# Kernel optimization log

Measured on AMD Instinct MI355X. Metric: run time of the kernel, lower is better.

The kernel has to match this reference:

```python
import jax, jax.numpy as jnp
import numpy as np

N_NODES = 100000


def gcn_conv(x, src, dst, W, b):
    # PyG GCNConv: linear transform first, then symmetric-normalized aggregation.
    h = x @ W  # [N, out]
    ones = jnp.ones(dst.shape[0], dtype=x.dtype)
    deg = jax.ops.segment_sum(ones, dst, num_segments=N_NODES)  # in-degree incl. self-loops
    dinv = jnp.where(deg > 0, jax.lax.rsqrt(deg), 0.0)
    norm = dinv[src] * dinv[dst]  # [E]
    msg = h[src] * norm[:, None]  # gather + scale
    out = jax.ops.segment_sum(msg, dst, num_segments=N_NODES)  # scatter-add
    return out + b


def add_self_loops(edge_index):
    loops = jnp.arange(N_NODES, dtype=edge_index.dtype)
    src = jnp.concatenate([edge_index[0], loops])
    dst = jnp.concatenate([edge_index[1], loops])
    return src, dst


def setup_inputs() -> dict:
    key = jax.random.key(0)
    k1, k2, k3, k4 = jax.random.split(key, 4)
    N, F, H, C, E = N_NODES, 512, 16, 40, 3200000
    x = jax.random.normal(k1, (N, F), dtype=jnp.float32)
    edge_index = jax.random.randint(k2, (2, E), 0, N, dtype=jnp.int64)
    W1 = jax.random.normal(k3, (F, H), dtype=jnp.float32) * (1.0 / np.sqrt(F))
    b1 = jnp.zeros((H,), dtype=jnp.float32)
    W2 = jax.random.normal(k4, (H, C), dtype=jnp.float32) * (1.0 / np.sqrt(H))
    b2 = jnp.zeros((C,), dtype=jnp.float32)
    return {"x": x, "edge_index": edge_index, "W1": W1, "b1": b1, "W2": W2, "b2": b2}


def reference(x, edge_index, W1, b1, W2, b2):
    src, dst = add_self_loops(edge_index)
    h = gcn_conv(x, src, dst, W1, b1)
    h = jax.nn.relu(h)
    logits = gcn_conv(h, src, dst, W2, b2)
    return jax.nn.log_softmax(logits, axis=1), logits
```

## Files before the change

### kernel.cpp

```cpp
#include <hip/hip_runtime.h>
#include <hip/hip_bf16.h>
#include <math.h>

#define N_NODES 100000
#define F_IN 512
#define H_DIM 16
#define C_DIM 40

#define BSHIFT 9
#define BNODES 512
#define NBUCK 196
#define CHUNK 8192
#define SRC_MASK 0x1FFFF
#define SORT_CAP 18432

#define KSPLIT 4
#define KSEG (F_IN / KSPLIT)


__global__ void __launch_bounds__(256) bhist_kernel(const int* __restrict__ dst,
                                                    int* __restrict__ BC, int E) {
    __shared__ int cnt[NBUCK];
    int start = blockIdx.x * CHUNK;
    int end = start + CHUNK < E ? start + CHUNK : E;
    for (int i = threadIdx.x; i < NBUCK; i += 256) cnt[i] = 0;
    __syncthreads();
    for (int i = start + threadIdx.x; i < end; i += 256)
        atomicAdd(&cnt[dst[i] >> BSHIFT], 1);
    __syncthreads();
    for (int i = threadIdx.x; i < NBUCK; i += 256) {
        int c = cnt[i];
        if (c) atomicAdd(&BC[i], c);
    }
}


__global__ void __launch_bounds__(256) bscan_kernel(const int* __restrict__ BC,
                                                    int* __restrict__ BO,
                                                    int* __restrict__ cursor,
                                                    int* __restrict__ R, int E, int N) {
    __shared__ int buf[2][256];
    int tid = threadIdx.x;
    int v = (tid < NBUCK) ? BC[tid] : 0;
    int cur = 0;
    buf[0][tid] = v;
    __syncthreads();
    for (int off = 1; off < 256; off <<= 1) {
        int t = buf[cur][tid] + ((tid >= off) ? buf[cur][tid - off] : 0);
        cur ^= 1;
        buf[cur][tid] = t;
        __syncthreads();
    }
    int excl = buf[cur][tid] - v;
    if (tid <= NBUCK) {
        BO[tid] = excl;
        if (tid < NBUCK) cursor[tid] = excl;
    }
    if (tid == 0) R[N] = E;
}


__global__ void __launch_bounds__(256) partition_kernel(const int* __restrict__ src,
                                                        const int* __restrict__ dst,
                                                        int* __restrict__ cursor,
                                                        int* __restrict__ packed, int E) {
    __shared__ int cnt[NBUCK];
    __shared__ int base[NBUCK];
    __shared__ int lpre[NBUCK + 1];
    __shared__ int sbuf[2][256];
    __shared__ int stage[CHUNK];
    int tid = threadIdx.x;
    int start = blockIdx.x * CHUNK;
    int end = start + CHUNK < E ? start + CHUNK : E;
    int nch = end - start;
    for (int i = tid; i < NBUCK; i += 256) cnt[i] = 0;
    __syncthreads();
    for (int i = start + tid; i < end; i += 256)
        atomicAdd(&cnt[dst[i] >> BSHIFT], 1);
    __syncthreads();
    int v = (tid < NBUCK) ? cnt[tid] : 0;
    int cur = 0;
    sbuf[0][tid] = v;
    __syncthreads();
    for (int off = 1; off < 256; off <<= 1) {
        int t = sbuf[cur][tid] + ((tid >= off) ? sbuf[cur][tid - off] : 0);
        cur ^= 1;
        sbuf[cur][tid] = t;
        __syncthreads();
    }
    if (tid < NBUCK) {
        lpre[tid] = sbuf[cur][tid] - v;
        base[tid] = v ? atomicAdd(&cursor[tid], v) : 0;
        cnt[tid] = 0;
    }
    if (tid == 0) lpre[NBUCK] = nch;
    __syncthreads();
    for (int i = start + tid; i < end; i += 256) {
        int d = dst[i];
        int b = d >> BSHIFT;
        int p = lpre[b] + atomicAdd(&cnt[b], 1);
        stage[p] = ((d & (BNODES - 1)) << 17) | src[i];
    }
    __syncthreads();
    for (int j = tid; j < nch; j += 256) {
        int loB = 0, hiB = NBUCK;
        while (hiB - loB > 1) {
            int mid = (loB + hiB) >> 1;
            if (lpre[mid] <= j) loB = mid; else hiB = mid;
        }
        packed[base[loB] + (j - lpre[loB])] = stage[j];
    }
}


__global__ void __launch_bounds__(1024) sort2_kernel(const int* __restrict__ BO,
                                                     const int* __restrict__ packed,
                                                     int* __restrict__ R,
                                                     float* __restrict__ dinv,
                                                     int* __restrict__ eidx, int N) {
    __shared__ int cnt[BNODES];
    __shared__ int buf[2][BNODES];
    __shared__ int stage[SORT_CAP];
    int b = blockIdx.x;
    int tid = threadIdx.x;
    int lo = BO[b], hi = BO[b + 1];
    int len = hi - lo;
    if (tid < BNODES) cnt[tid] = 0;
    __syncthreads();
    for (int e = lo + tid; e < hi; e += 1024)
        atomicAdd(&cnt[packed[e] >> 17], 1);
    __syncthreads();
    int deg = (tid < BNODES) ? cnt[tid] : 0;
    int cur = 0;
    if (tid < BNODES) buf[0][tid] = deg;
    __syncthreads();
    for (int off = 1; off < BNODES; off <<= 1) {
        int t = 0;
        if (tid < BNODES) t = buf[cur][tid] + ((tid >= off) ? buf[cur][tid - off] : 0);
        cur ^= 1;
        if (tid < BNODES) buf[cur][tid] = t;
        __syncthreads();
    }
    if (tid < BNODES) {
        int excl = buf[cur][tid] - deg;
        int n = (b << BSHIFT) + tid;
        if (n < N) {
            R[n] = lo + excl;
            dinv[n] = rsqrtf((float)(deg + 1));
        }
        cnt[tid] = excl;
    }
    __syncthreads();
    if (len <= SORT_CAP) {
        for (int e = lo + tid; e < hi; e += 1024) {
            int p = packed[e];
            int pos = atomicAdd(&cnt[p >> 17], 1);
            stage[pos] = p & SRC_MASK;
        }
        __syncthreads();
        for (int j = tid; j < len; j += 1024) eidx[lo + j] = stage[j];
    } else {
        for (int e = lo + tid; e < hi; e += 1024) {
            int p = packed[e];
            int pos = atomicAdd(&cnt[p >> 17], 1);
            eidx[lo + pos] = p & SRC_MASK;
        }
    }
}


#define G1_ISSUE(BUF, G)                                             \
    {                                                                \
        _Pragma("unroll")                                            \
        for (int p = 0; p < 8; ++p) BUF[p] = xr[(G) * 8 + p];        \
    }

#define G1_COMPUTE(BUF, G)                                           \
    {                                                                \
        const float* xf = (const float*)(BUF);                       \
        _Pragma("unroll")                                            \
        for (int j = 0; j < 32; ++j) {                               \
            float s = xf[j];                                         \
            const float4* Wj = (const float4*)(Wb + ((G) * 32 + j) * H_DIM); \
            _Pragma("unroll")                                        \
            for (int p = 0; p < 4; ++p) {                            \
                float4 wv = Wj[p];                                   \
                acc[4 * p + 0] += s * wv.x;                          \
                acc[4 * p + 1] += s * wv.y;                          \
                acc[4 * p + 2] += s * wv.z;                          \
                acc[4 * p + 3] += s * wv.w;                          \
            }                                                        \
        }                                                            \
    }

__global__ void __launch_bounds__(256) gemm1p_kernel(const float* __restrict__ x,
                                                     const float* __restrict__ W1,
                                                     float* __restrict__ part, int N) {
    int bid = blockIdx.x;
    int ks = bid & (KSPLIT - 1);
    int rb = bid >> 2;
    int row = rb * 256 + threadIdx.x;
    int cr = row < N ? row : N - 1;
    const float4* xr = (const float4*)(x + (size_t)cr * F_IN + ks * KSEG);
    const float* Wb = W1 + ks * KSEG * H_DIM;

    float4 bufA[8], bufB[8];
    float acc[H_DIM];
#pragma unroll
    for (int k = 0; k < H_DIM; k++) acc[k] = 0.0f;

    G1_ISSUE(bufA, 0);
    G1_ISSUE(bufB, 1);
    G1_COMPUTE(bufA, 0);
    G1_ISSUE(bufA, 2);
    G1_COMPUTE(bufB, 1);
    G1_ISSUE(bufB, 3);
    G1_COMPUTE(bufA, 2);
    G1_COMPUTE(bufB, 3);

    if (row < N) {
        float4* o = (float4*)(part + (size_t)ks * N * H_DIM + (size_t)row * H_DIM);
#pragma unroll
        for (int p = 0; p < 4; p++)
            o[p] = make_float4(acc[4 * p], acc[4 * p + 1], acc[4 * p + 2], acc[4 * p + 3]);
    }
}


__global__ void __launch_bounds__(256) g1red_kernel(const float* __restrict__ part,
                                                    const float* __restrict__ dinv,
                                                    float* __restrict__ g1, int N) {
    int t = blockIdx.x * 256 + threadIdx.x;
    int total = N * H_DIM / 4;
    if (t >= total) return;
    const float4* p = (const float4*)part;
    float4 a = p[t];
    float4 b = p[t + (size_t)total];
    float4 c = p[t + (size_t)2 * total];
    float4 d = p[t + (size_t)3 * total];
    float di = dinv[t >> 2];
    ((float4*)g1)[t] = make_float4(di * (((a.x + b.x) + c.x) + d.x),
                                   di * (((a.y + b.y) + c.y) + d.y),
                                   di * (((a.z + b.z) + c.z) + d.z),
                                   di * (((a.w + b.w) + c.w) + d.w));
}


__global__ void __launch_bounds__(256) agg1_kernel(const int* __restrict__ R,
                                                   const int* __restrict__ eidx,
                                                   const float* __restrict__ g1,
                                                   const float* __restrict__ dinv,
                                                   const float* __restrict__ b1,
                                                   float* __restrict__ g2, int N) {
    int t = blockIdx.x * 256 + threadIdx.x;
    int n = t >> 4;
    if (n >= N) return;
    int k = t & 15;
    int lo = R[n], hi = R[n + 1];
    float sum = g1[t];
    int e = lo;
    for (; e + 8 <= hi; e += 8) {
        int s[8];
        float v[8];
#pragma unroll
        for (int u = 0; u < 8; u++) s[u] = eidx[e + u];
#pragma unroll
        for (int u = 0; u < 8; u++) v[u] = g1[s[u] * H_DIM + k];
#pragma unroll
        for (int u = 0; u < 8; u++) sum += v[u];
    }
    for (; e < hi; ++e) sum += g1[eidx[e] * H_DIM + k];
    float di = dinv[n];
    g2[t] = di * fmaxf(di * sum + b1[k], 0.0f);
}


__global__ void __launch_bounds__(256) fin2_kernel(const int* __restrict__ R,
                                                   const int* __restrict__ eidx,
                                                   const float* __restrict__ g2,
                                                   const float* __restrict__ dinv,
                                                   const float* __restrict__ W2,
                                                   const float* __restrict__ b2,
                                                   float* __restrict__ out, int N) {
    __shared__ float w2s[H_DIM * C_DIM];
    __shared__ float b2s[C_DIM];
    __shared__ float vsh[16][17];
    for (int i = threadIdx.x; i < H_DIM * C_DIM; i += 256) w2s[i] = W2[i];
    if (threadIdx.x < C_DIM) b2s[threadIdx.x] = b2[threadIdx.x];

    int t = blockIdx.x * 256 + threadIdx.x;
    int n = t >> 4;
    int k = t & 15;
    int lo = R[n], hi = R[n + 1];
    float sum = g2[t];
    int e = lo;
    for (; e + 8 <= hi; e += 8) {
        int s[8];
        float v[8];
#pragma unroll
        for (int u = 0; u < 8; u++) s[u] = eidx[e + u];
#pragma unroll
        for (int u = 0; u < 8; u++) v[u] = g2[s[u] * H_DIM + k];
#pragma unroll
        for (int u = 0; u < 8; u++) sum += v[u];
    }
    for (; e < hi; ++e) sum += g2[eidx[e] * H_DIM + k];
    vsh[threadIdx.x >> 4][k] = dinv[n] * sum;
    __syncthreads();

    int g = threadIdx.x >> 4;
    int j = threadIdx.x & 15;
    const float* v = vsh[g];
    int c2 = (j < 8) ? 32 + j : j;
    float lg0 = b2s[j];
    float lg1 = b2s[j + 16];
    float lg2 = (j < 8) ? b2s[32 + j] : -1e30f;
    float lg2acc = 0.0f;
#pragma unroll
    for (int kk = 0; kk < H_DIM; ++kk) {
        float vk = v[kk];
        lg0 += vk * w2s[kk * C_DIM + j];
        lg1 += vk * w2s[kk * C_DIM + j + 16];
        lg2acc += vk * w2s[kk * C_DIM + c2];
    }
    if (j < 8) lg2 += lg2acc;

    float m = fmaxf(fmaxf(lg0, lg1), lg2);
#pragma unroll
    for (int s = 1; s < 16; s <<= 1) m = fmaxf(m, __shfl_xor(m, s, 64));
    float ss = __expf(lg0 - m) + __expf(lg1 - m) + ((j < 8) ? __expf(lg2 - m) : 0.0f);
#pragma unroll
    for (int s = 1; s < 16; s <<= 1) ss += __shfl_xor(ss, s, 64);
    float lse = m + __logf(ss);

    size_t base = (size_t)n * C_DIM;
    size_t lim = (size_t)N * C_DIM;
    out[base + j] = lg0 - lse;
    out[base + 16 + j] = lg1 - lse;
    if (j < 8) out[base + 32 + j] = lg2 - lse;
    out[lim + base + j] = lg0;
    out[lim + base + 16 + j] = lg1;
    if (j < 8) out[lim + base + 32 + j] = lg2;
}


extern "C" void kernel_launch(void* const* d_in, const int* in_sizes, int n_in,
                              void* d_out, int out_size, void* d_ws, size_t ws_size,
                              hipStream_t stream) {
    const float* x  = (const float*)d_in[0];
    const int* ei   = (const int*)d_in[1];
    const float* W1 = (const float*)d_in[2];
    const float* b1 = (const float*)d_in[3];
    const float* W2 = (const float*)d_in[4];
    const float* b2 = (const float*)d_in[5];
    float* out = (float*)d_out;

    const int N = N_NODES;
    const int E = in_sizes[1] / 2;
    const int* src = ei;
    const int* dst = ei + E;

    int* R      = (int*)d_ws;
    int* BC     = R + 100016;
    int* BO     = BC + 512;
    int* cursor = BO + 256;
    float* dinv = (float*)(cursor + 256);
    int* eidx   = (int*)(dinv + 100016);
    int* packed = eidx + E;
    float* g1   = (float*)packed;
    float* g2   = g1 + 16 * N;
    float* part = g2 + 16 * N;

    const int NB = (N + 255) / 256;
    const int NCH = (E + CHUNK - 1) / CHUNK;

    hipMemsetAsync(BC, 0, NBUCK * sizeof(int), stream);
    bhist_kernel<<<NCH, 256, 0, stream>>>(dst, BC, E);
    bscan_kernel<<<1, 256, 0, stream>>>(BC, BO, cursor, R, E, N);
    partition_kernel<<<NCH, 256, 0, stream>>>(src, dst, cursor, packed, E);
    sort2_kernel<<<NBUCK, 1024, 0, stream>>>(BO, packed, R, dinv, eidx, N);

    gemm1p_kernel<<<NB * KSPLIT, 256, 0, stream>>>(x, W1, part, N);
    g1red_kernel<<<(N * H_DIM / 4 + 255) / 256, 256, 0, stream>>>(part, dinv, g1, N);
    agg1_kernel<<<(N * 16 + 255) / 256, 256, 0, stream>>>(R, eidx, g1, dinv, b1, g2, N);
    fin2_kernel<<<N / 16, 256, 0, stream>>>(R, eidx, g2, dinv, W2, b2, out, N);
}
```

Baseline: 518.2 us.

## Merge partition with GEMM and sort with reduction, using fixed-capacity buckets

Drops the separate histogram and scan passes by giving each destination bucket a fixed-capacity region (CAP slots), so the partition step can claim offsets directly through atomic cursors. The partition and the x@W1 split-K GEMM now run as one launch using disjoint block ranges, and the per-bucket sort is fused with the partial-sum reduction, so independent work overlaps and the launch count drops. Because dinv is no longer ready when g1 is reduced, agg1 now gathers dinv per neighbour and applies it there, and R2 stores explicit row ends since rows are no longer contiguous. The cost is an extra dinv gather per edge in agg1 and a silent correctness risk if any bucket receives more edges than CAP.

```diff
diff --git a/kernel.cpp b/kernel.cpp
--- a/kernel.cpp
+++ b/kernel.cpp
@@ -10,163 +10,13 @@
 #define BSHIFT 9
 #define BNODES 512
 #define NBUCK 196
-#define CHUNK 8192
+#define CHUNK4 4096
 #define SRC_MASK 0x1FFFF
+#define CAP 20480
 #define SORT_CAP 18432
 
 #define KSPLIT 4
 #define KSEG (F_IN / KSPLIT)
-
-
-__global__ void __launch_bounds__(256) bhist_kernel(const int* __restrict__ dst,
-                                                    int* __restrict__ BC, int E) {
-    __shared__ int cnt[NBUCK];
-    int start = blockIdx.x * CHUNK;
-    int end = start + CHUNK < E ? start + CHUNK : E;
-    for (int i = threadIdx.x; i < NBUCK; i += 256) cnt[i] = 0;
-    __syncthreads();
-    for (int i = start + threadIdx.x; i < end; i += 256)
-        atomicAdd(&cnt[dst[i] >> BSHIFT], 1);
-    __syncthreads();
-    for (int i = threadIdx.x; i < NBUCK; i += 256) {
-        int c = cnt[i];
-        if (c) atomicAdd(&BC[i], c);
-    }
-}
-
-
-__global__ void __launch_bounds__(256) bscan_kernel(const int* __restrict__ BC,
-                                                    int* __restrict__ BO,
-                                                    int* __restrict__ cursor,
-                                                    int* __restrict__ R, int E, int N) {
-    __shared__ int buf[2][256];
-    int tid = threadIdx.x;
-    int v = (tid < NBUCK) ? BC[tid] : 0;
-    int cur = 0;
-    buf[0][tid] = v;
-    __syncthreads();
-    for (int off = 1; off < 256; off <<= 1) {
-        int t = buf[cur][tid] + ((tid >= off) ? buf[cur][tid - off] : 0);
-        cur ^= 1;
-        buf[cur][tid] = t;
-        __syncthreads();
-    }
-    int excl = buf[cur][tid] - v;
-    if (tid <= NBUCK) {
-        BO[tid] = excl;
-        if (tid < NBUCK) cursor[tid] = excl;
-    }
-    if (tid == 0) R[N] = E;
-}
-
-
-__global__ void __launch_bounds__(256) partition_kernel(const int* __restrict__ src,
-                                                        const int* __restrict__ dst,
-                                                        int* __restrict__ cursor,
-                                                        int* __restrict__ packed, int E) {
-    __shared__ int cnt[NBUCK];
-    __shared__ int base[NBUCK];
-    __shared__ int lpre[NBUCK + 1];
-    __shared__ int sbuf[2][256];
-    __shared__ int stage[CHUNK];
-    int tid = threadIdx.x;
-    int start = blockIdx.x * CHUNK;
-    int end = start + CHUNK < E ? start + CHUNK : E;
-    int nch = end - start;
-    for (int i = tid; i < NBUCK; i += 256) cnt[i] = 0;
-    __syncthreads();
-    for (int i = start + tid; i < end; i += 256)
-        atomicAdd(&cnt[dst[i] >> BSHIFT], 1);
-    __syncthreads();
-    int v = (tid < NBUCK) ? cnt[tid] : 0;
-    int cur = 0;
-    sbuf[0][tid] = v;
-    __syncthreads();
-    for (int off = 1; off < 256; off <<= 1) {
-        int t = sbuf[cur][tid] + ((tid >= off) ? sbuf[cur][tid - off] : 0);
-        cur ^= 1;
-        sbuf[cur][tid] = t;
-        __syncthreads();
-    }
-    if (tid < NBUCK) {
-        lpre[tid] = sbuf[cur][tid] - v;
-        base[tid] = v ? atomicAdd(&cursor[tid], v) : 0;
-        cnt[tid] = 0;
-    }
-    if (tid == 0) lpre[NBUCK] = nch;
-    __syncthreads();
-    for (int i = start + tid; i < end; i += 256) {
-        int d = dst[i];
-        int b = d >> BSHIFT;
-        int p = lpre[b] + atomicAdd(&cnt[b], 1);
-        stage[p] = ((d & (BNODES - 1)) << 17) | src[i];
-    }
-    __syncthreads();
-    for (int j = tid; j < nch; j += 256) {
-        int loB = 0, hiB = NBUCK;
-        while (hiB - loB > 1) {
-            int mid = (loB + hiB) >> 1;
-            if (lpre[mid] <= j) loB = mid; else hiB = mid;
-        }
-        packed[base[loB] + (j - lpre[loB])] = stage[j];
-    }
-}
-
-
-__global__ void __launch_bounds__(1024) sort2_kernel(const int* __restrict__ BO,
-                                                     const int* __restrict__ packed,
-                                                     int* __restrict__ R,
-                                                     float* __restrict__ dinv,
-                                                     int* __restrict__ eidx, int N) {
-    __shared__ int cnt[BNODES];
-    __shared__ int buf[2][BNODES];
-    __shared__ int stage[SORT_CAP];
-    int b = blockIdx.x;
-    int tid = threadIdx.x;
-    int lo = BO[b], hi = BO[b + 1];
-    int len = hi - lo;
-    if (tid < BNODES) cnt[tid] = 0;
-    __syncthreads();
-    for (int e = lo + tid; e < hi; e += 1024)
-        atomicAdd(&cnt[packed[e] >> 17], 1);
-    __syncthreads();
-    int deg = (tid < BNODES) ? cnt[tid] : 0;
-    int cur = 0;
-    if (tid < BNODES) buf[0][tid] = deg;
-    __syncthreads();
-    for (int off = 1; off < BNODES; off <<= 1) {
-        int t = 0;
-        if (tid < BNODES) t = buf[cur][tid] + ((tid >= off) ? buf[cur][tid - off] : 0);
-        cur ^= 1;
-        if (tid < BNODES) buf[cur][tid] = t;
-        __syncthreads();
-    }
-    if (tid < BNODES) {
-        int excl = buf[cur][tid] - deg;
-        int n = (b << BSHIFT) + tid;
-        if (n < N) {
-            R[n] = lo + excl;
-            dinv[n] = rsqrtf((float)(deg + 1));
-        }
-        cnt[tid] = excl;
-    }
-    __syncthreads();
-    if (len <= SORT_CAP) {
-        for (int e = lo + tid; e < hi; e += 1024) {
-            int p = packed[e];
-            int pos = atomicAdd(&cnt[p >> 17], 1);
-            stage[pos] = p & SRC_MASK;
-        }
-        __syncthreads();
-        for (int j = tid; j < len; j += 1024) eidx[lo + j] = stage[j];
-    } else {
-        for (int e = lo + tid; e < hi; e += 1024) {
-            int p = packed[e];
-            int pos = atomicAdd(&cnt[p >> 17], 1);
-            eidx[lo + pos] = p & SRC_MASK;
-        }
-    }
-}
 
 
 #define G1_ISSUE(BUF, G)                                             \
@@ -193,60 +43,175 @@
         }                                                            \
     }
 
-__global__ void __launch_bounds__(256) gemm1p_kernel(const float* __restrict__ x,
-                                                     const float* __restrict__ W1,
-                                                     float* __restrict__ part, int N) {
-    int bid = blockIdx.x;
-    int ks = bid & (KSPLIT - 1);
-    int rb = bid >> 2;
-    int row = rb * 256 + threadIdx.x;
-    int cr = row < N ? row : N - 1;
-    const float4* xr = (const float4*)(x + (size_t)cr * F_IN + ks * KSEG);
-    const float* Wb = W1 + ks * KSEG * H_DIM;
-
-    float4 bufA[8], bufB[8];
-    float acc[H_DIM];
-#pragma unroll
-    for (int k = 0; k < H_DIM; k++) acc[k] = 0.0f;
-
-    G1_ISSUE(bufA, 0);
-    G1_ISSUE(bufB, 1);
-    G1_COMPUTE(bufA, 0);
-    G1_ISSUE(bufA, 2);
-    G1_COMPUTE(bufB, 1);
-    G1_ISSUE(bufB, 3);
-    G1_COMPUTE(bufA, 2);
-    G1_COMPUTE(bufB, 3);
-
-    if (row < N) {
-        float4* o = (float4*)(part + (size_t)ks * N * H_DIM + (size_t)row * H_DIM);
-#pragma unroll
-        for (int p = 0; p < 4; p++)
-            o[p] = make_float4(acc[4 * p], acc[4 * p + 1], acc[4 * p + 2], acc[4 * p + 3]);
-    }
-}
-
-
-__global__ void __launch_bounds__(256) g1red_kernel(const float* __restrict__ part,
-                                                    const float* __restrict__ dinv,
-                                                    float* __restrict__ g1, int N) {
-    int t = blockIdx.x * 256 + threadIdx.x;
-    int total = N * H_DIM / 4;
-    if (t >= total) return;
-    const float4* p = (const float4*)part;
-    float4 a = p[t];
-    float4 b = p[t + (size_t)total];
-    float4 c = p[t + (size_t)2 * total];
-    float4 d = p[t + (size_t)3 * total];
-    float di = dinv[t >> 2];
-    ((float4*)g1)[t] = make_float4(di * (((a.x + b.x) + c.x) + d.x),
-                                   di * (((a.y + b.y) + c.y) + d.y),
-                                   di * (((a.z + b.z) + c.z) + d.z),
-                                   di * (((a.w + b.w) + c.w) + d.w));
+__global__ void __launch_bounds__(256) k1_kernel(const int* __restrict__ src,
+                                                 const int* __restrict__ dst,
+                                                 int* __restrict__ cursor,
+                                                 int* __restrict__ packed,
+                                                 const float* __restrict__ x,
+                                                 const float* __restrict__ W1,
+                                                 float* __restrict__ part,
+                                                 int E, int N, int NCH4) {
+    __shared__ int cnt[NBUCK];
+    __shared__ int base[NBUCK];
+    __shared__ int lpre[NBUCK + 1];
+    __shared__ int sbuf[2][256];
+    __shared__ int stage[CHUNK4];
+
+    if ((int)blockIdx.x < NCH4) {
+        int tid = threadIdx.x;
+        int start = blockIdx.x * CHUNK4;
+        int end = start + CHUNK4 < E ? start + CHUNK4 : E;
+        int nch = end - start;
+        for (int i = tid; i < NBUCK; i += 256) cnt[i] = 0;
+        __syncthreads();
+        for (int i = start + tid; i < end; i += 256)
+            atomicAdd(&cnt[dst[i] >> BSHIFT], 1);
+        __syncthreads();
+        int v = (tid < NBUCK) ? cnt[tid] : 0;
+        int cur = 0;
+        sbuf[0][tid] = v;
+        __syncthreads();
+        for (int off = 1; off < 256; off <<= 1) {
+            int t = sbuf[cur][tid] + ((tid >= off) ? sbuf[cur][tid - off] : 0);
+            cur ^= 1;
+            sbuf[cur][tid] = t;
+            __syncthreads();
+        }
+        if (tid < NBUCK) {
+            lpre[tid] = sbuf[cur][tid] - v;
+            base[tid] = tid * CAP + (v ? atomicAdd(&cursor[tid], v) : 0);
+            cnt[tid] = 0;
+        }
+        if (tid == 0) lpre[NBUCK] = nch;
+        __syncthreads();
+        for (int i = start + tid; i < end; i += 256) {
+            int d = dst[i];
+            int b = d >> BSHIFT;
+            int p = lpre[b] + atomicAdd(&cnt[b], 1);
+            stage[p] = ((d & (BNODES - 1)) << 17) | src[i];
+        }
+        __syncthreads();
+        for (int j = tid; j < nch; j += 256) {
+            int loB = 0, hiB = NBUCK;
+            while (hiB - loB > 1) {
+                int mid = (loB + hiB) >> 1;
+                if (lpre[mid] <= j) loB = mid; else hiB = mid;
+            }
+            packed[base[loB] + (j - lpre[loB])] = stage[j];
+        }
+    } else {
+        int bid = blockIdx.x - NCH4;
+        int ks = bid & (KSPLIT - 1);
+        int rb = bid >> 2;
+        int row = rb * 256 + threadIdx.x;
+        int cr = row < N ? row : N - 1;
+        const float4* xr = (const float4*)(x + (size_t)cr * F_IN + ks * KSEG);
+        const float* Wb = W1 + ks * KSEG * H_DIM;
+
+        float4 bufA[8], bufB[8];
+        float acc[H_DIM];
+#pragma unroll
+        for (int k = 0; k < H_DIM; k++) acc[k] = 0.0f;
+
+        G1_ISSUE(bufA, 0);
+        G1_ISSUE(bufB, 1);
+        G1_COMPUTE(bufA, 0);
+        G1_ISSUE(bufA, 2);
+        G1_COMPUTE(bufB, 1);
+        G1_ISSUE(bufB, 3);
+        G1_COMPUTE(bufA, 2);
+        G1_COMPUTE(bufB, 3);
+
+        if (row < N) {
+            float4* o = (float4*)(part + (size_t)ks * N * H_DIM + (size_t)row * H_DIM);
+#pragma unroll
+            for (int p = 0; p < 4; p++)
+                o[p] = make_float4(acc[4 * p], acc[4 * p + 1], acc[4 * p + 2], acc[4 * p + 3]);
+        }
+    }
+}
+
+
+__global__ void __launch_bounds__(1024) k2_kernel(const int* __restrict__ cursor,
+                                                  const int* __restrict__ packed,
+                                                  int* __restrict__ R,
+                                                  int* __restrict__ R2,
+                                                  float* __restrict__ dinv,
+                                                  int* __restrict__ eidx,
+                                                  const float* __restrict__ part,
+                                                  float* __restrict__ g1, int N) {
+    __shared__ int cnt[BNODES];
+    __shared__ int buf[2][BNODES];
+    __shared__ int stage[SORT_CAP];
+
+    if (blockIdx.x < NBUCK) {
+        int b = blockIdx.x;
+        int tid = threadIdx.x;
+        int lo = b * CAP;
+        int len = cursor[b];
+        int hi = lo + len;
+        if (tid < BNODES) cnt[tid] = 0;
+        __syncthreads();
+        for (int e = lo + tid; e < hi; e += 1024)
+            atomicAdd(&cnt[packed[e] >> 17], 1);
+        __syncthreads();
+        int deg = (tid < BNODES) ? cnt[tid] : 0;
+        int cur = 0;
+        if (tid < BNODES) buf[0][tid] = deg;
+        __syncthreads();
+        for (int off = 1; off < BNODES; off <<= 1) {
+            int t = 0;
+            if (tid < BNODES) t = buf[cur][tid] + ((tid >= off) ? buf[cur][tid - off] : 0);
+            cur ^= 1;
+            if (tid < BNODES) buf[cur][tid] = t;
+            __syncthreads();
+        }
+        if (tid < BNODES) {
+            int excl = buf[cur][tid] - deg;
+            int n = (b << BSHIFT) + tid;
+            if (n < N) {
+                R[n] = lo + excl;
+                R2[n] = lo + excl + deg;
+                dinv[n] = rsqrtf((float)(deg + 1));
+            }
+            cnt[tid] = excl;
+        }
+        __syncthreads();
+        if (len <= SORT_CAP) {
+            for (int e = lo + tid; e < hi; e += 1024) {
+                int p = packed[e];
+                int pos = atomicAdd(&cnt[p >> 17], 1);
+                stage[pos] = p & SRC_MASK;
+            }
+            __syncthreads();
+            for (int j = tid; j < len; j += 1024) eidx[lo + j] = stage[j];
+        } else {
+            for (int e = lo + tid; e < hi; e += 1024) {
+                int p = packed[e];
+                int pos = atomicAdd(&cnt[p >> 17], 1);
+                eidx[lo + pos] = p & SRC_MASK;
+            }
+        }
+    } else {
+        int t = (blockIdx.x - NBUCK) * 1024 + threadIdx.x;
+        int total = N * H_DIM / 4;
+        if (t < total) {
+            const float4* p = (const float4*)part;
+            float4 a = p[t];
+            float4 b = p[t + (size_t)total];
+            float4 c = p[t + (size_t)2 * total];
+            float4 d = p[t + (size_t)3 * total];
+            ((float4*)g1)[t] = make_float4((((a.x + b.x) + c.x) + d.x),
+                                           (((a.y + b.y) + c.y) + d.y),
+                                           (((a.z + b.z) + c.z) + d.z),
+                                           (((a.w + b.w) + c.w) + d.w));
+        }
+    }
 }
 
 
 __global__ void __launch_bounds__(256) agg1_kernel(const int* __restrict__ R,
+                                                   const int* __restrict__ R2,
                                                    const int* __restrict__ eidx,
                                                    const float* __restrict__ g1,
                                                    const float* __restrict__ dinv,
@@ -256,26 +221,33 @@
     int n = t >> 4;
     if (n >= N) return;
     int k = t & 15;
-    int lo = R[n], hi = R[n + 1];
-    float sum = g1[t];
+    int lo = R[n], hi = R2[n];
+    float di = dinv[n];
+    float sum = di * g1[t];
     int e = lo;
     for (; e + 8 <= hi; e += 8) {
         int s[8];
+        float dv[8];
         float v[8];
 #pragma unroll
         for (int u = 0; u < 8; u++) s[u] = eidx[e + u];
 #pragma unroll
+        for (int u = 0; u < 8; u++) dv[u] = dinv[s[u]];
+#pragma unroll
         for (int u = 0; u < 8; u++) v[u] = g1[s[u] * H_DIM + k];
 #pragma unroll
-        for (int u = 0; u < 8; u++) sum += v[u];
-    }
-    for (; e < hi; ++e) sum += g1[eidx[e] * H_DIM + k];
-    float di = dinv[n];
+        for (int u = 0; u < 8; u++) sum += v[u] * dv[u];
+    }
+    for (; e < hi; ++e) {
+        int s = eidx[e];
+        sum += g1[s * H_DIM + k] * dinv[s];
+    }
     g2[t] = di * fmaxf(di * sum + b1[k], 0.0f);
 }
 
 
 __global__ void __launch_bounds__(256) fin2_kernel(const int* __restrict__ R,
+                                                   const int* __restrict__ R2,
                                                    const int* __restrict__ eidx,
                                                    const float* __restrict__ g2,
                                                    const float* __restrict__ dinv,
@@ -291,7 +263,7 @@
     int t = blockIdx.x * 256 + threadIdx.x;
     int n = t >> 4;
     int k = t & 15;
-    int lo = R[n], hi = R[n + 1];
+    int lo = R[n], hi = R2[n];
     float sum = g2[t];
     int e = lo;
     for (; e + 8 <= hi; e += 8) {
@@ -361,27 +333,23 @@
     const int* dst = ei + E;
 
     int* R      = (int*)d_ws;
-    int* BC     = R + 100016;
-    int* BO     = BC + 512;
-    int* cursor = BO + 256;
+    int* R2     = R + 100016;
+    int* cursor = R2 + 100016;
     float* dinv = (float*)(cursor + 256);
     int* eidx   = (int*)(dinv + 100016);
-    int* packed = eidx + E;
-    float* g1   = (float*)packed;
+    int* packed = eidx + NBUCK * CAP;
+    float* g1   = (float*)(packed + NBUCK * CAP);
     float* g2   = g1 + 16 * N;
     float* part = g2 + 16 * N;
 
     const int NB = (N + 255) / 256;
-    const int NCH = (E + CHUNK - 1) / CHUNK;
-
-    hipMemsetAsync(BC, 0, NBUCK * sizeof(int), stream);
-    bhist_kernel<<<NCH, 256, 0, stream>>>(dst, BC, E);
-    bscan_kernel<<<1, 256, 0, stream>>>(BC, BO, cursor, R, E, N);
-    partition_kernel<<<NCH, 256, 0, stream>>>(src, dst, cursor, packed, E);
-    sort2_kernel<<<NBUCK, 1024, 0, stream>>>(BO, packed, R, dinv, eidx, N);
-
-    gemm1p_kernel<<<NB * KSPLIT, 256, 0, stream>>>(x, W1, part, N);
-    g1red_kernel<<<(N * H_DIM / 4 + 255) / 256, 256, 0, stream>>>(part, dinv, g1, N);
-    agg1_kernel<<<(N * 16 + 255) / 256, 256, 0, stream>>>(R, eidx, g1, dinv, b1, g2, N);
-    fin2_kernel<<<N / 16, 256, 0, stream>>>(R, eidx, g2, dinv, W2, b2, out, N);
-}
+    const int NCH4 = (E + CHUNK4 - 1) / CHUNK4;
+
+    hipMemsetAsync(cursor, 0, NBUCK * sizeof(int), stream);
+    k1_kernel<<<NCH4 + NB * KSPLIT, 256, 0, stream>>>(src, dst, cursor, packed,
+                                                      x, W1, part, E, N, NCH4);
+    k2_kernel<<<NBUCK + (N * H_DIM / 4 + 1023) / 1024, 1024, 0, stream>>>(
+        cursor, packed, R, R2, dinv, eidx, part, g1, N);
+    agg1_kernel<<<(N * 16 + 255) / 256, 256, 0, stream>>>(R, R2, eidx, g1, dinv, b1, g2, N);
+    fin2_kernel<<<N / 16, 256, 0, stream>>>(R, R2, eidx, g2, dinv, W2, b2, out, N);
+}
```

New measurement: 483.2 us. 6.7% less time.
